# Kernel optimization log

Measured on AMD Instinct MI355X. Metric: run time of the kernel, lower is better.

Reference implementation:

```python
import jax, jax.numpy as jnp
import numpy as np

HID = 256   # hidden_dim
P = 16      # pool_size
EPS = 1e-5


def _ln(x, g, b):
    m = x.mean(-1, keepdims=True)
    v = x.var(-1, keepdims=True)
    return (x - m) * jax.lax.rsqrt(v + EPS) * g + b


def setup_inputs() -> dict:
    key = jax.random.key(0)
    ks = jax.random.split(key, 12)
    B, Cf, H, W = 8, 512, 64, 64
    Cg = Cf // 2
    Co = Cf // 2
    s = 0.02
    d = {}
    d['e_f'] = jax.random.normal(ks[0], (B, Cf, H, W), jnp.float32)
    d['e_g'] = jax.random.normal(ks[1], (B, Cg, H, W), jnp.float32)
    d['l_feat'] = jax.random.normal(ks[2], (B, 768, 20), jnp.float32)
    d['l_mask'] = jnp.ones((B, 20, 1), jnp.float32)
    d['ln_f_g'] = jnp.ones((Cf,), jnp.float32)
    d['ln_f_b'] = jnp.zeros((Cf,), jnp.float32)
    d['ln_g_g'] = jnp.ones((Cg,), jnp.float32)
    d['ln_g_b'] = jnp.zeros((Cg,), jnp.float32)
    d['wq'] = jax.random.normal(ks[3], (Cf, HID), jnp.float32) * s
    d['bq'] = jnp.zeros((HID,), jnp.float32)
    d['wk'] = jax.random.normal(ks[4], (Cg, HID), jnp.float32) * s
    d['bk'] = jnp.zeros((HID,), jnp.float32)
    d['wv'] = jax.random.normal(ks[5], (Cg, HID), jnp.float32) * s
    d['bv'] = jnp.zeros((HID,), jnp.float32)
    d['wo'] = jax.random.normal(ks[6], (HID, HID), jnp.float32) * s
    d['bo'] = jnp.zeros((HID,), jnp.float32)
    d['dw_k'] = jax.random.normal(ks[7], (HID, 1, 3, 3), jnp.float32) * s  # depthwise kernel (OIHW, I=1)
    d['efp_w'] = jax.random.normal(ks[8], (HID, Cf), jnp.float32) * s     # 1x1 conv v_channels->hidden
    d['efp_b'] = jnp.zeros((HID,), jnp.float32)
    d['outc_w'] = jax.random.normal(ks[9], (Co, HID), jnp.float32) * s    # 1x1 conv hidden->out
    d['outc_b'] = jnp.zeros((Co,), jnp.float32)
    d['bn_g'] = jnp.ones((Co,), jnp.float32)
    d['bn_b'] = jnp.zeros((Co,), jnp.float32)
    d['bn_m'] = jnp.zeros((Co,), jnp.float32)
    d['bn_v'] = jnp.ones((Co,), jnp.float32)
    return d


def reference(e_f, e_g, l_feat, l_mask, ln_f_g, ln_f_b, ln_g_g, ln_g_b,
              wq, bq, wk, bk, wv, bv, wo, bo, dw_k, efp_w, efp_b,
              outc_w, outc_b, bn_g, bn_b, bn_m, bn_v):
    B, Cf, H, W = e_f.shape
    # Q = w_qi(LN(e_f))                                  (B, HW, HID)
    q = _ln(e_f.transpose(0, 2, 3, 1), ln_f_g, ln_f_b).reshape(B, H * W, Cf) @ wq + bq
    # K/V projections from LN(e_g)
    g = _ln(e_g.transpose(0, 2, 3, 1), ln_g_g, ln_g_b).reshape(B, H * W, -1)
    k = (g @ wk + bk).reshape(B, H, W, HID)
    v = (g @ wv + bv).reshape(B, H, W, HID)
    # 16x16 max/avg pooling -> (B, Hp*Wp, HID)
    k = jnp.max(k.reshape(B, H // P, P, W // P, P, HID), axis=(2, 4)).reshape(B, -1, HID)
    v = jnp.mean(v.reshape(B, H // P, P, W // P, P, HID), axis=(2, 4)).reshape(B, -1, HID)
    # pooled attention
    attn = jax.nn.softmax(jnp.einsum('bqd,bkd->bqk', q, k) * (HID ** -0.5), axis=-1)
    a_i = jnp.einsum('bqk,bkd->bqd', attn, v)  # (B, HW, HID)
    # depthwise 3x3 conv on Q (NCHW)
    q_nchw = q.reshape(B, H, W, HID).transpose(0, 3, 1, 2)
    dw = jax.lax.conv_general_dilated(q_nchw, dw_k, (1, 1), [(1, 1), (1, 1)],
                                      feature_group_count=HID)
    combined = dw + a_i.reshape(B, H, W, HID).transpose(0, 3, 1, 2)
    comb = combined.transpose(0, 2, 3, 1).reshape(B, H * W, HID) @ wo + bo
    comb = comb.reshape(B, H, W, HID).transpose(0, 3, 1, 2)
    # 1x1 proj of e_f, elementwise gate
    efp = jnp.einsum('bchw,oc->bohw', e_f, efp_w) + efp_b[None, :, None, None]
    e_a = efp * comb
    # out: 1x1 conv + BN (inference) + ReLU (dropout inactive in eval)
    out = jnp.einsum('bchw,oc->bohw', e_a, outc_w) + outc_b[None, :, None, None]
    scale = (bn_g * jax.lax.rsqrt(bn_v + EPS))[None, :, None, None]
    out = (out - bn_m[None, :, None, None]) * scale + bn_b[None, :, None, None]
    return jax.nn.relu(out)
```

## Files before the change

### kernel.cpp

```cpp
#include <hip/hip_runtime.h>
#include <math.h>

#define EPS 1e-5f

typedef __attribute__((ext_vector_type(8))) short bf16x8;
typedef __attribute__((ext_vector_type(4))) float f32x4;

__device__ __forceinline__ unsigned short f2bf(float f) {
    unsigned int u = __float_as_uint(f);
    u += 0x7fff + ((u >> 16) & 1);
    return (unsigned short)(u >> 16);
}
__device__ __forceinline__ float bf2f(unsigned short h) {
    return __uint_as_float(((unsigned int)h) << 16);
}
__device__ __forceinline__ float lof(unsigned int u) {
    return __uint_as_float(u << 16);
}
__device__ __forceinline__ float hif(unsigned int u) {
    return __uint_as_float(u & 0xffff0000u);
}
__device__ __forceinline__ void async16(void* lds, const void* g) {
    __builtin_amdgcn_global_load_lds(
        (const __attribute__((address_space(1))) unsigned int*)g,
        (__attribute__((address_space(3))) unsigned int*)lds, 16, 0, 0);
}

__global__ __launch_bounds__(256) void prep_all(
    const float* __restrict__ lnfg, const float* __restrict__ lnfb,
    const float* __restrict__ wq, const float* __restrict__ bq,
    const float* __restrict__ efpw, const float* __restrict__ efpb,
    const float* __restrict__ lngg, const float* __restrict__ lngb,
    const float* __restrict__ wk, const float* __restrict__ bk,
    const float* __restrict__ wv, const float* __restrict__ bv,
    const float* __restrict__ wo, const float* __restrict__ outcw,
    const float* __restrict__ outcb, const float* __restrict__ bng,
    const float* __restrict__ bnb, const float* __restrict__ bnm,
    const float* __restrict__ bnv, const float* __restrict__ dwk,
    unsigned short* __restrict__ Wb1t, unsigned short* __restrict__ Wb2t,
    unsigned short* __restrict__ Wot, unsigned short* __restrict__ Woc,
    float* __restrict__ dwt,
    float* __restrict__ cs1, float* __restrict__ cst1,
    float* __restrict__ cs2, float* __restrict__ cst2,
    float* __restrict__ scv, float* __restrict__ shv)
{
    int idx = blockIdx.x * 256 + threadIdx.x;
    if (idx < 262144) {
        int n = idx >> 9, k = idx & 511;
        float v = (n < 256) ? lnfg[k] * wq[k * 256 + n]
                            : efpw[(size_t)(n - 256) * 512 + k];
        Wb1t[idx] = f2bf(v);
    } else if (idx < 327680) {
        int j = idx - 262144; int n = j >> 8, k = j & 255;
        Wb2t[j] = f2bf(lngg[k] * wk[k * 256 + n]);
    } else if (idx < 393216) {
        int j = idx - 327680; int n = j >> 8, k = j & 255;
        Wot[j] = f2bf(wo[k * 256 + n]);
    } else if (idx < 458752) {
        int j = idx - 393216;
        Woc[j] = f2bf(outcw[j]);
    } else if (idx < 461056) {
        int j = idx - 458752; int tap = j >> 8, ch = j & 255;
        dwt[j] = dwk[ch * 9 + tap];
    } else if (idx < 462336) {
        int j = idx - 461056;
        if (j < 256) {
            int n = j; float cs = 0.f, ct = 0.f;
            for (int k = 0; k < 512; k++) {
                float w = wq[k * 256 + n];
                cs += lnfg[k] * w; ct += lnfb[k] * w;
            }
            cs1[n] = cs; cst1[n] = ct + bq[n];
        } else if (j < 512) {
            cs1[j] = 0.f; cst1[j] = efpb[j - 256];
        } else if (j < 768) {
            int n = j - 512; float cs = 0.f, ct = 0.f;
            for (int k = 0; k < 256; k++) {
                float w = wk[k * 256 + n];
                cs += lngg[k] * w; ct += lngb[k] * w;
            }
            cs2[n] = cs; cst2[n] = ct + bk[n];
        } else if (j < 1024) {
            int n = j - 768; float cs = 0.f, ct = 0.f;
            for (int k = 0; k < 256; k++) {
                float w = wv[k * 256 + n];
                cs += lngg[k] * w; ct += lngb[k] * w;
            }
            cs2[256 + n] = cs; cst2[256 + n] = ct + bv[n];
        } else {
            int n = j - 1024;
            float s = bng[n] * rsqrtf(bnv[n] + EPS);
            scv[n] = s;
            shv[n] = (outcb[n] - bnm[n]) * s + bnb[n];
        }
    }
}

__global__ __launch_bounds__(256) void transpose_fg(
    const float* __restrict__ ef, const float* __restrict__ eg,
    unsigned short* __restrict__ ef_bf, unsigned short* __restrict__ eg_bf,
    float* __restrict__ pf, float* __restrict__ pfq,
    float* __restrict__ pg, float* __restrict__ pgq)
{
    __shared__ float tile[64][65];
    __shared__ float psum[4][64], pss[4][64];
    int id = blockIdx.x;
    const float* src; unsigned short* dst; float* ps; float* pq;
    int C, cblk, b, p0;
    if (id < 2048) {
        src = ef; dst = ef_bf; ps = pf; pq = pfq; C = 512;
        b = id >> 8; cblk = (id >> 5) & 7; p0 = (id & 31) * 128;
    } else {
        id -= 2048;
        src = eg; dst = eg_bf; ps = pg; pq = pgq; C = 256;
        b = id >> 7; cblk = (id >> 5) & 3; p0 = (id & 31) * 128;
    }
    int c0 = cblk * 64;
    const float* s = src + ((size_t)b * C + c0) * 4096 + p0;
    int t = threadIdx.x;
    int cr = t >> 4, p4 = (t & 15) * 4;
    int lane = t & 63, grp = t >> 6;
    int pr = t >> 3, c8 = (t & 7) * 8;

    float4 r1[4], r2[4];
#pragma unroll
    for (int i = 0; i < 4; i++)
        r1[i] = *(const float4*)(s + (size_t)(i * 16 + cr) * 4096 + p4);
#pragma unroll
    for (int i = 0; i < 4; i++)
        r2[i] = *(const float4*)(s + (size_t)(i * 16 + cr) * 4096 + 64 + p4);

#pragma unroll
    for (int half = 0; half < 2; half++) {
#pragma unroll
        for (int i = 0; i < 4; i++) {
            float4 v = half ? r2[i] : r1[i];
            int c = i * 16 + cr;
            tile[c][p4 + 0] = v.x; tile[c][p4 + 1] = v.y;
            tile[c][p4 + 2] = v.z; tile[c][p4 + 3] = v.w;
        }
        __syncthreads();

        int pbase = p0 + half * 64;
        unsigned short* d = dst + ((size_t)(b * 4096 + pbase)) * C + c0;
#pragma unroll
        for (int i = 0; i < 2; i++) {
            int p = i * 32 + pr;
            uint4 pk;
            pk.x = (unsigned)f2bf(tile[c8 + 0][p]) | ((unsigned)f2bf(tile[c8 + 1][p]) << 16);
            pk.y = (unsigned)f2bf(tile[c8 + 2][p]) | ((unsigned)f2bf(tile[c8 + 3][p]) << 16);
            pk.z = (unsigned)f2bf(tile[c8 + 4][p]) | ((unsigned)f2bf(tile[c8 + 5][p]) << 16);
            pk.w = (unsigned)f2bf(tile[c8 + 6][p]) | ((unsigned)f2bf(tile[c8 + 7][p]) << 16);
            *(uint4*)(d + (size_t)p * C + c8) = pk;
        }

        float sm = 0.f, sq = 0.f;
#pragma unroll
        for (int j = 0; j < 16; j++) {
            float v = tile[grp * 16 + j][lane];
            sm += v; sq += v * v;
        }
        psum[grp][lane] = sm; pss[grp][lane] = sq;
        __syncthreads();
        if (t < 64) {
            float fs = psum[0][t] + psum[1][t] + psum[2][t] + psum[3][t];
            float fq = pss[0][t] + pss[1][t] + pss[2][t] + pss[3][t];
            ps[cblk * 32768 + b * 4096 + pbase + t] = fs;
            pq[cblk * 32768 + b * 4096 + pbase + t] = fq;
        }
        if (half == 0) __syncthreads();
    }
}

__global__ __launch_bounds__(256) void ln_finalize(
    const float* __restrict__ pf, const float* __restrict__ pfq,
    const float* __restrict__ pg, const float* __restrict__ pgq,
    float* __restrict__ mf, float* __restrict__ rf,
    float* __restrict__ mg, float* __restrict__ rg)
{
    int gp = blockIdx.x * 256 + threadIdx.x;
    float s = 0.f, q = 0.f;
#pragma unroll
    for (int i = 0; i < 8; i++) { s += pf[i * 32768 + gp]; q += pfq[i * 32768 + gp]; }
    float m = s * (1.f / 512.f);
    float v = q * (1.f / 512.f) - m * m;
    mf[gp] = m; rf[gp] = rsqrtf(v + EPS);
    s = 0.f; q = 0.f;
#pragma unroll
    for (int i = 0; i < 4; i++) { s += pg[i * 32768 + gp]; q += pgq[i * 32768 + gp]; }
    m = s * (1.f / 256.f);
    v = q * (1.f / 256.f) - m * m;
    mg[gp] = m; rg[gp] = rsqrtf(v + EPS);
}

template<int K>
__device__ __forceinline__ void mfma_core(
    const unsigned short* __restrict__ A, const unsigned short* __restrict__ Bt,
    int m0, int n0, unsigned short* As, unsigned short* Bs, f32x4 acc[4][4])
{
    const int tid = threadIdx.x;
    const int wave = tid >> 6, lane = tid & 63;
    const int wm = (wave & 1) * 64, wn = (wave >> 1) * 64;
#pragma unroll
    for (int i = 0; i < 4; i++)
#pragma unroll
        for (int j = 0; j < 4; j++) acc[i][j] = (f32x4){0.f, 0.f, 0.f, 0.f};

    const int srow = wave * 32 + (lane >> 3);
    const int sg = (lane & 7) ^ ((lane >> 3) & 7);
    const unsigned short* ga = A + (size_t)(m0 + srow) * K + sg * 8;
    const unsigned short* gb = Bt + (size_t)(n0 + srow) * K + sg * 8;

    for (int k0 = 0; k0 < K; k0 += 64) {
#pragma unroll
        for (int t = 0; t < 4; t++) {
            async16(As + (wave * 32 + t * 8) * 64, ga + (size_t)t * 8 * K + k0);
            async16(Bs + (wave * 32 + t * 8) * 64, gb + (size_t)t * 8 * K + k0);
        }
        __syncthreads();
#pragma unroll
        for (int ks = 0; ks < 2; ks++) {
            bf16x8 af[4], bfr[4];
            int kb = ks * 4 + (lane >> 4);
            int slot = (kb ^ (lane & 7)) * 8;
#pragma unroll
            for (int i = 0; i < 4; i++) {
                int m = wm + i * 16 + (lane & 15);
                af[i] = *(const bf16x8*)&As[m * 64 + slot];
                int n = wn + i * 16 + (lane & 15);
                bfr[i] = *(const bf16x8*)&Bs[n * 64 + slot];
            }
#pragma unroll
            for (int i = 0; i < 4; i++)
#pragma unroll
                for (int j = 0; j < 4; j++)
                    acc[i][j] = __builtin_amdgcn_mfma_f32_16x16x32_bf16(
                        af[i], bfr[j], acc[i][j], 0, 0, 0);
        }
        __syncthreads();
    }
}

__global__ __launch_bounds__(256, 2) void gemm1_mfma(
    const unsigned short* __restrict__ ef_bf, const unsigned short* __restrict__ Wb1t,
    const float* __restrict__ cs1, const float* __restrict__ cst1,
    const float* __restrict__ mf, const float* __restrict__ rf,
    unsigned short* __restrict__ qbuf, unsigned short* __restrict__ efpbuf)
{
    __shared__ unsigned short As[128 * 64];
    __shared__ unsigned short Bs[256 * 64];
    f32x4 acc[4][8];
    const int tid = threadIdx.x;
    const int wave = tid >> 6, lane = tid & 63;
    const int wm = (wave & 1) * 64, wn = (wave >> 1) * 128;
    const int m0 = blockIdx.x * 128, n0 = blockIdx.y * 256;
#pragma unroll
    for (int i = 0; i < 4; i++)
#pragma unroll
        for (int j = 0; j < 8; j++) acc[i][j] = (f32x4){0.f, 0.f, 0.f, 0.f};

    const int srow = lane >> 3;
    const int sg = (lane & 7) ^ (srow & 7);
    const unsigned short* ga = ef_bf + (size_t)(m0 + wave * 32 + srow) * 512 + sg * 8;
    const unsigned short* gb = Wb1t + (size_t)(n0 + wave * 64 + srow) * 512 + sg * 8;

    for (int k0 = 0; k0 < 512; k0 += 64) {
#pragma unroll
        for (int t = 0; t < 4; t++)
            async16(As + (wave * 32 + t * 8) * 64, ga + (size_t)t * 8 * 512 + k0);
#pragma unroll
        for (int t = 0; t < 8; t++)
            async16(Bs + (wave * 64 + t * 8) * 64, gb + (size_t)t * 8 * 512 + k0);
        __syncthreads();
#pragma unroll
        for (int ks = 0; ks < 2; ks++) {
            bf16x8 af[4], bfr[8];
            int kb = ks * 4 + (lane >> 4);
            int slot = (kb ^ (lane & 7)) * 8;
#pragma unroll
            for (int i = 0; i < 4; i++)
                af[i] = *(const bf16x8*)&As[(wm + i * 16 + (lane & 15)) * 64 + slot];
#pragma unroll
            for (int j = 0; j < 8; j++)
                bfr[j] = *(const bf16x8*)&Bs[(wn + j * 16 + (lane & 15)) * 64 + slot];
#pragma unroll
            for (int i = 0; i < 4; i++)
#pragma unroll
                for (int j = 0; j < 8; j++)
                    acc[i][j] = __builtin_amdgcn_mfma_f32_16x16x32_bf16(
                        af[i], bfr[j], acc[i][j], 0, 0, 0);
        }
        __syncthreads();
    }

    bool isq = (n0 == 0);
#pragma unroll
    for (int i = 0; i < 4; i++) {
#pragma unroll
        for (int r = 0; r < 4; r++) {
            int gm = m0 + wm + i * 16 + ((lane >> 4) * 4) + r;
            float mean = mf[gm], rs = rf[gm];
#pragma unroll
            for (int j = 0; j < 8; j++) {
                int nn = wn + j * 16 + (lane & 15);
                float v = acc[i][j][r];
                if (isq) {
                    int n = nn;
                    float o = rs * (v - mean * cs1[n]) + cst1[n];
                    qbuf[(size_t)gm * 256 + nn] = f2bf(o);
                } else {
                    int n = nn + 256;
                    efpbuf[(size_t)gm * 256 + nn] = f2bf(v + cst1[n]);
                }
            }
        }
    }
}

__global__ __launch_bounds__(256) void gemm2k_mfma(
    const unsigned short* __restrict__ eg_bf, const unsigned short* __restrict__ Wb2t,
    const float* __restrict__ cs2, const float* __restrict__ cst2,
    const float* __restrict__ mg, const float* __restrict__ rg,
    unsigned short* __restrict__ kfull)
{
    __shared__ unsigned short As[8192], Bs[8192];
    f32x4 acc[4][4];
    int m0 = blockIdx.x * 128, n0 = blockIdx.y * 128;
    mfma_core<256>(eg_bf, Wb2t, m0, n0, As, Bs, acc);
    int lane = threadIdx.x & 63, wave = threadIdx.x >> 6;
    int wm = (wave & 1) * 64, wn = (wave >> 1) * 64;
#pragma unroll
    for (int i = 0; i < 4; i++) {
#pragma unroll
        for (int r = 0; r < 4; r++) {
            int gm = m0 + wm + i * 16 + ((lane >> 4) * 4) + r;
            float mean = mg[gm], rs = rg[gm];
#pragma unroll
            for (int j = 0; j < 4; j++) {
                int n = n0 + wn + j * 16 + (lane & 15);
                float o = rs * (acc[i][j][r] - mean * cs2[n]) + cst2[n];
                kfull[(size_t)gm * 256 + n] = f2bf(o);
            }
        }
    }
}

__global__ __launch_bounds__(256) void gemm34_mfma(
    const unsigned short* __restrict__ comb, const unsigned short* __restrict__ Wot,
    const float* __restrict__ bo, const unsigned short* __restrict__ efp,
    const unsigned short* __restrict__ Woc,
    const float* __restrict__ scv, const float* __restrict__ shv,
    float* __restrict__ outp)
{
    __shared__ unsigned short As[64 * 64];
    __shared__ unsigned short Bs[256 * 64];
    __shared__ unsigned short eat[64 * 256];
    const int tid = threadIdx.x;
    const int wave = tid >> 6, lane = tid & 63;
    const int m0 = blockIdx.x * 64;

    const int srow = lane >> 3;
    const int sg = (lane & 7) ^ (srow & 7);

    f32x4 acc[4][4];
#pragma unroll
    for (int i = 0; i < 4; i++)
#pragma unroll
        for (int j = 0; j < 4; j++) acc[i][j] = (f32x4){0.f, 0.f, 0.f, 0.f};

    const unsigned short* ga = comb + (size_t)(m0 + wave * 16 + srow) * 256 + sg * 8;
    const unsigned short* gb = Wot + (size_t)(wave * 64 + srow) * 256 + sg * 8;

    for (int k0 = 0; k0 < 256; k0 += 64) {
#pragma unroll
        for (int t = 0; t < 2; t++)
            async16(As + (wave * 16 + t * 8) * 64, ga + (size_t)t * 8 * 256 + k0);
#pragma unroll
        for (int t = 0; t < 8; t++)
            async16(Bs + (wave * 64 + t * 8) * 64, gb + (size_t)t * 8 * 256 + k0);
        __syncthreads();
#pragma unroll
        for (int ks = 0; ks < 2; ks++) {
            bf16x8 af[4], bfr[4];
            int kb = ks * 4 + (lane >> 4);
            int slot = (kb ^ (lane & 7)) * 8;
#pragma unroll
            for (int i = 0; i < 4; i++) {
                af[i]  = *(const bf16x8*)&As[(i * 16 + (lane & 15)) * 64 + slot];
                bfr[i] = *(const bf16x8*)&Bs[(wave * 64 + i * 16 + (lane & 15)) * 64 + slot];
            }
#pragma unroll
            for (int i = 0; i < 4; i++)
#pragma unroll
                for (int j = 0; j < 4; j++)
                    acc[i][j] = __builtin_amdgcn_mfma_f32_16x16x32_bf16(
                        af[i], bfr[j], acc[i][j], 0, 0, 0);
        }
        __syncthreads();
    }

    float bo4[4];
#pragma unroll
    for (int j = 0; j < 4; j++) bo4[j] = bo[wave * 64 + j * 16 + (lane & 15)];
#pragma unroll
    for (int i = 0; i < 4; i++) {
#pragma unroll
        for (int r = 0; r < 4; r++) {
            int pos = i * 16 + ((lane >> 4) * 4) + r;
#pragma unroll
            for (int j = 0; j < 4; j++) {
                int n = wave * 64 + j * 16 + (lane & 15);
                float o = (acc[i][j][r] + bo4[j])
                          * bf2f(efp[(size_t)(m0 + pos) * 256 + n]);
                int o8 = j * 2 + ((lane >> 3) & 1);
                int slot = o8 ^ (pos & 7);
                eat[pos * 256 + wave * 64 + slot * 8 + (lane & 7)] = f2bf(o);
            }
        }
    }

    f32x4 acc2[4][4];
#pragma unroll
    for (int i = 0; i < 4; i++)
#pragma unroll
        for (int j = 0; j < 4; j++) acc2[i][j] = (f32x4){0.f, 0.f, 0.f, 0.f};

    const unsigned short* gw = Woc + (size_t)(wave * 64 + srow) * 256 + sg * 8;
    for (int k0 = 0; k0 < 256; k0 += 64) {
#pragma unroll
        for (int t = 0; t < 8; t++)
            async16(Bs + (wave * 64 + t * 8) * 64, gw + (size_t)t * 8 * 256 + k0);
        __syncthreads();
        int kc = k0 >> 6;
#pragma unroll
        for (int ks = 0; ks < 2; ks++) {
            bf16x8 af2[4], bf2_[4];
            int kb = ks * 4 + (lane >> 4);
            int slot = (kb ^ (lane & 7)) * 8;
#pragma unroll
            for (int i = 0; i < 4; i++) {
                af2[i]  = *(const bf16x8*)&Bs[(wave * 64 + i * 16 + (lane & 15)) * 64 + slot];
                bf2_[i] = *(const bf16x8*)&eat[(i * 16 + (lane & 15)) * 256 + kc * 64 + slot];
            }
#pragma unroll
            for (int i = 0; i < 4; i++)
#pragma unroll
                for (int j = 0; j < 4; j++)
                    acc2[i][j] = __builtin_amdgcn_mfma_f32_16x16x32_bf16(
                        af2[i], bf2_[j], acc2[i][j], 0, 0, 0);
        }
        __syncthreads();
    }

#pragma unroll
    for (int i = 0; i < 4; i++) {
#pragma unroll
        for (int r = 0; r < 4; r++) {
            int co = wave * 64 + i * 16 + ((lane >> 4) * 4) + r;
            float s = scv[co], hh = shv[co];
#pragma unroll
            for (int j = 0; j < 4; j++) {
                int p = m0 + j * 16 + (lane & 15);
                float o = fmaxf(fmaf(acc2[i][j][r], s, hh), 0.f);
                outp[((size_t)(p >> 12)) * 1048576 + (size_t)co * 4096 + (p & 4095)] = o;
            }
        }
    }
}

__global__ __launch_bounds__(256) void pool_phase(
    const unsigned short* __restrict__ kfull, const float* __restrict__ eg,
    const float* __restrict__ rg, const float* __restrict__ mg,
    unsigned short* __restrict__ kpb, float* __restrict__ s1,
    float* __restrict__ s0)
{
    __shared__ float smem[4352];
    int id = blockIdx.x;
    int t = threadIdx.x;
    if (id < 128) {
        int b = id >> 4, cell = id & 15;
        int hp = cell >> 2, wp = cell & 3;
        int g8 = t & 31, rr = t >> 5;
        float kmx[8];
#pragma unroll
        for (int j = 0; j < 8; j++) kmx[j] = -3.402823466e38f;
#pragma unroll
        for (int rsub = 0; rsub < 2; rsub++) {
            int r = rr * 2 + rsub;
            int prow = (hp * 16 + r) * 64 + wp * 16;
            for (int cl = 0; cl < 16; cl++) {
                size_t basei = ((size_t)(b * 4096 + prow + cl)) * 256 + g8 * 8;
                uint4 kv = *(const uint4*)(kfull + basei);
                kmx[0] = fmaxf(kmx[0], lof(kv.x)); kmx[1] = fmaxf(kmx[1], hif(kv.x));
                kmx[2] = fmaxf(kmx[2], lof(kv.y)); kmx[3] = fmaxf(kmx[3], hif(kv.y));
                kmx[4] = fmaxf(kmx[4], lof(kv.z)); kmx[5] = fmaxf(kmx[5], hif(kv.z));
                kmx[6] = fmaxf(kmx[6], lof(kv.w)); kmx[7] = fmaxf(kmx[7], hif(kv.w));
            }
// ... 129 lines not shown
        int hh = h + dy - 1;
        if (hh < 0 || hh > 63) continue;
        const unsigned short* qr = qbuf + ((size_t)(b * 4096 + hh * 64)) * 256;
        float4 ft[6];
#pragma unroll
        for (int c = 0; c < 6; c++) {
            int xx = w0 - 1 + c;
            if (xx < 0 || xx > 63) {
                ft[c] = (float4){0.f, 0.f, 0.f, 0.f};
            } else {
                uint2 qa = *(const uint2*)(qr + (size_t)xx * 256 + o4);
                ft[c] = (float4){lof(qa.x), hif(qa.x), lof(qa.y), hif(qa.y)};
            }
        }
#pragma unroll
        for (int dx = 0; dx < 3; dx++) {
            float4 kk = kreg[dy * 3 + dx];
#pragma unroll
            for (int i = 0; i < 4; i++) {
                float4 qv = ft[i + dx];
                acc[i].x = fmaf(qv.x, kk.x, acc[i].x);
                acc[i].y = fmaf(qv.y, kk.y, acc[i].y);
                acc[i].z = fmaf(qv.z, kk.z, acc[i].z);
                acc[i].w = fmaf(qv.w, kk.w, acc[i].w);
            }
        }
    }
#pragma unroll
    for (int i = 0; i < 4; i++) {
        uint2 pk;
        pk.x = (unsigned)f2bf(acc[i].x) | ((unsigned)f2bf(acc[i].y) << 16);
        pk.y = (unsigned)f2bf(acc[i].z) | ((unsigned)f2bf(acc[i].w) << 16);
        *(uint2*)(combined + ((size_t)(b * 4096 + pidx + i)) * 256 + o4) = pk;
    }
}

extern "C" void kernel_launch(void* const* d_in, const int* in_sizes, int n_in,
                              void* d_out, int out_size, void* d_ws, size_t ws_size,
                              hipStream_t stream)
{
    const float* e_f   = (const float*)d_in[0];
    const float* e_g   = (const float*)d_in[1];
    const float* lnfg  = (const float*)d_in[4];
    const float* lnfb  = (const float*)d_in[5];
    const float* lngg  = (const float*)d_in[6];
    const float* lngb  = (const float*)d_in[7];
    const float* wq    = (const float*)d_in[8];
    const float* bq    = (const float*)d_in[9];
    const float* wk    = (const float*)d_in[10];
    const float* bk    = (const float*)d_in[11];
    const float* wv    = (const float*)d_in[12];
    const float* bv    = (const float*)d_in[13];
    const float* wo    = (const float*)d_in[14];
    const float* bo    = (const float*)d_in[15];
    const float* dwk   = (const float*)d_in[16];
    const float* efpw  = (const float*)d_in[17];
    const float* efpb  = (const float*)d_in[18];
    const float* outcw = (const float*)d_in[19];
    const float* outcb = (const float*)d_in[20];
    const float* bng   = (const float*)d_in[21];
    const float* bnb   = (const float*)d_in[22];
    const float* bnm   = (const float*)d_in[23];
    const float* bnv   = (const float*)d_in[24];
    float* outp = (float*)d_out;

    char* base = (char*)d_ws;
    auto alloc = [&](size_t bytes) -> char* {
        char* r = base; base += (bytes + 255) & ~(size_t)255; return r;
    };
    float* pf    = (float*)alloc(8 * 32768 * 4);
    float* pfq   = (float*)alloc(8 * 32768 * 4);
    float* pg    = (float*)alloc(4 * 32768 * 4);
    float* pgq   = (float*)alloc(4 * 32768 * 4);
    float* mf    = (float*)alloc(32768 * 4);
    float* rf    = (float*)alloc(32768 * 4);
    float* mg    = (float*)alloc(32768 * 4);
    float* rg    = (float*)alloc(32768 * 4);
    float* cs1   = (float*)alloc(512 * 4);
    float* cst1  = (float*)alloc(512 * 4);
    float* cs2   = (float*)alloc(512 * 4);
    float* cst2  = (float*)alloc(512 * 4);
    float* scv   = (float*)alloc(256 * 4);
    float* shv   = (float*)alloc(256 * 4);
    float* dwt   = (float*)alloc(9 * 256 * 4);
    unsigned short* Wb1t = (unsigned short*)alloc(262144 * 2);
    unsigned short* Wb2t = (unsigned short*)alloc(65536 * 2);
    unsigned short* Wot  = (unsigned short*)alloc(65536 * 2);
    unsigned short* Woc  = (unsigned short*)alloc(65536 * 2);
    unsigned short* ef_bf = (unsigned short*)alloc((size_t)32768 * 512 * 2);
    unsigned short* eg_bf = (unsigned short*)alloc((size_t)32768 * 256 * 2);
    unsigned short* qbuf  = (unsigned short*)alloc((size_t)32768 * 256 * 2);
    unsigned short* efpbuf = (unsigned short*)alloc((size_t)32768 * 256 * 2);
    unsigned short* kfull = (unsigned short*)alloc((size_t)32768 * 256 * 2);
    unsigned short* kpb  = (unsigned short*)alloc(128 * 256 * 2);
    float* vp    = (float*)alloc(128 * 256 * 4);
    float* s1    = (float*)alloc(128 * 256 * 4);
    float* s0    = (float*)alloc(128 * 4);

    prep_all<<<1806, 256, 0, stream>>>(
        lnfg, lnfb, wq, bq, efpw, efpb, lngg, lngb, wk, bk, wv, bv, wo,
        outcw, outcb, bng, bnb, bnm, bnv, dwk,
        Wb1t, Wb2t, Wot, Woc, dwt, cs1, cst1, cs2, cst2, scv, shv);
    transpose_fg<<<3072, 256, 0, stream>>>(e_f, e_g, ef_bf, eg_bf,
                                           pf, pfq, pg, pgq);
    ln_finalize<<<128, 256, 0, stream>>>(pf, pfq, pg, pgq, mf, rf, mg, rg);
    gemm1_mfma<<<dim3(256, 2), 256, 0, stream>>>(ef_bf, Wb1t, cs1, cst1, mf, rf,
                                                 qbuf, efpbuf);
    gemm2k_mfma<<<dim3(256, 2), 256, 0, stream>>>(eg_bf, Wb2t, cs2, cst2, mg, rg,
                                                  kfull);
    pool_phase<<<640, 256, 0, stream>>>(kfull, e_g, rg, mg, kpb, s1, s0);
    vpool_gemm<<<128, 256, 0, stream>>>(s1, s0, lngg, wv, cs2, cst2, vp);
    combined_dw<<<2048, 256, 0, stream>>>(qbuf, kpb, vp, dwt, kfull);
    gemm34_mfma<<<512, 256, 0, stream>>>(kfull, Wot, bo, efpbuf,
                                         Woc, scv, shv, outp);
}
```

Measured before the change: 316.7 us.

## Merge prep with transpose, fold LN finalize into GEMMs, and merge projection GEMMs

Weight prep and the input transpose/stat pass now run in a single launch with block-index dispatch. The separate LN-finalize kernel is removed: each projection GEMM block reduces the partial sums for its own rows into shared memory, and the K-GEMM still writes mg/rg for later kernels. The Q/efp GEMM and the K GEMM are merged into one 1024-block launch. This saves launches and inter-kernel gaps, at the cost of a fatter kernel whose register and LDS use is sized for the heavier branch.

Measured after the change: 311.5 us. No clear change (-1.7%).

```diff
diff --git a/kernel.cpp b/kernel.cpp
--- a/kernel.cpp
+++ b/kernel.cpp
@@ -26,7 +26,11 @@
         (__attribute__((address_space(3))) unsigned int*)lds, 16, 0, 0);
 }
 
-__global__ __launch_bounds__(256) void prep_all(
+__global__ __launch_bounds__(256) void trans_prep(
+    const float* __restrict__ ef, const float* __restrict__ eg,
+    unsigned short* __restrict__ ef_bf, unsigned short* __restrict__ eg_bf,
+    float* __restrict__ pf, float* __restrict__ pfq,
+    float* __restrict__ pg, float* __restrict__ pgq,
     const float* __restrict__ lnfg, const float* __restrict__ lnfb,
     const float* __restrict__ wq, const float* __restrict__ bq,
     const float* __restrict__ efpw, const float* __restrict__ efpb,
@@ -44,153 +48,127 @@
     float* __restrict__ cs2, float* __restrict__ cst2,
     float* __restrict__ scv, float* __restrict__ shv)
 {
-    int idx = blockIdx.x * 256 + threadIdx.x;
-    if (idx < 262144) {
-        int n = idx >> 9, k = idx & 511;
-        float v = (n < 256) ? lnfg[k] * wq[k * 256 + n]
-                            : efpw[(size_t)(n - 256) * 512 + k];
-        Wb1t[idx] = f2bf(v);
-    } else if (idx < 327680) {
-        int j = idx - 262144; int n = j >> 8, k = j & 255;
-        Wb2t[j] = f2bf(lngg[k] * wk[k * 256 + n]);
-    } else if (idx < 393216) {
-        int j = idx - 327680; int n = j >> 8, k = j & 255;
-        Wot[j] = f2bf(wo[k * 256 + n]);
-    } else if (idx < 458752) {
-        int j = idx - 393216;
-        Woc[j] = f2bf(outcw[j]);
-    } else if (idx < 461056) {
-        int j = idx - 458752; int tap = j >> 8, ch = j & 255;
-        dwt[j] = dwk[ch * 9 + tap];
-    } else if (idx < 462336) {
-        int j = idx - 461056;
-        if (j < 256) {
-            int n = j; float cs = 0.f, ct = 0.f;
-            for (int k = 0; k < 512; k++) {
-                float w = wq[k * 256 + n];
-                cs += lnfg[k] * w; ct += lnfb[k] * w;
-            }
-            cs1[n] = cs; cst1[n] = ct + bq[n];
-        } else if (j < 512) {
-            cs1[j] = 0.f; cst1[j] = efpb[j - 256];
-        } else if (j < 768) {
-            int n = j - 512; float cs = 0.f, ct = 0.f;
-            for (int k = 0; k < 256; k++) {
-                float w = wk[k * 256 + n];
-                cs += lngg[k] * w; ct += lngb[k] * w;
-            }
-            cs2[n] = cs; cst2[n] = ct + bk[n];
-        } else if (j < 1024) {
-            int n = j - 768; float cs = 0.f, ct = 0.f;
-            for (int k = 0; k < 256; k++) {
-                float w = wv[k * 256 + n];
-                cs += lngg[k] * w; ct += lngb[k] * w;
-            }
-            cs2[256 + n] = cs; cst2[256 + n] = ct + bv[n];
-        } else {
-            int n = j - 1024;
-            float s = bng[n] * rsqrtf(bnv[n] + EPS);
-            scv[n] = s;
-            shv[n] = (outcb[n] - bnm[n]) * s + bnb[n];
-        }
-    }
-}
-
-__global__ __launch_bounds__(256) void transpose_fg(
-    const float* __restrict__ ef, const float* __restrict__ eg,
-    unsigned short* __restrict__ ef_bf, unsigned short* __restrict__ eg_bf,
-    float* __restrict__ pf, float* __restrict__ pfq,
-    float* __restrict__ pg, float* __restrict__ pgq)
-{
     __shared__ float tile[64][65];
     __shared__ float psum[4][64], pss[4][64];
     int id = blockIdx.x;
-    const float* src; unsigned short* dst; float* ps; float* pq;
-    int C, cblk, b, p0;
-    if (id < 2048) {
-        src = ef; dst = ef_bf; ps = pf; pq = pfq; C = 512;
-        b = id >> 8; cblk = (id >> 5) & 7; p0 = (id & 31) * 128;
+    if (id < 3072) {
+        const float* src; unsigned short* dst; float* ps; float* pq;
+        int C, cblk, b, p0;
+        if (id < 2048) {
+            src = ef; dst = ef_bf; ps = pf; pq = pfq; C = 512;
+            b = id >> 8; cblk = (id >> 5) & 7; p0 = (id & 31) * 128;
+        } else {
+            id -= 2048;
+            src = eg; dst = eg_bf; ps = pg; pq = pgq; C = 256;
+            b = id >> 7; cblk = (id >> 5) & 3; p0 = (id & 31) * 128;
+        }
+        int c0 = cblk * 64;
+        const float* s = src + ((size_t)b * C + c0) * 4096 + p0;
+        int t = threadIdx.x;
+        int cr = t >> 4, p4 = (t & 15) * 4;
+        int lane = t & 63, grp = t >> 6;
+        int pr = t >> 3, c8 = (t & 7) * 8;
+
+        float4 r1[4], r2[4];
+#pragma unroll
+        for (int i = 0; i < 4; i++)
+            r1[i] = *(const float4*)(s + (size_t)(i * 16 + cr) * 4096 + p4);
+#pragma unroll
+        for (int i = 0; i < 4; i++)
+            r2[i] = *(const float4*)(s + (size_t)(i * 16 + cr) * 4096 + 64 + p4);
+
+#pragma unroll
+        for (int half = 0; half < 2; half++) {
+#pragma unroll
+            for (int i = 0; i < 4; i++) {
+                float4 v = half ? r2[i] : r1[i];
+                int c = i * 16 + cr;
+                tile[c][p4 + 0] = v.x; tile[c][p4 + 1] = v.y;
+                tile[c][p4 + 2] = v.z; tile[c][p4 + 3] = v.w;
+            }
+            __syncthreads();
+
+            int pbase = p0 + half * 64;
+            unsigned short* d = dst + ((size_t)(b * 4096 + pbase)) * C + c0;
+#pragma unroll
+            for (int i = 0; i < 2; i++) {
+                int p = i * 32 + pr;
+                uint4 pk;
+                pk.x = (unsigned)f2bf(tile[c8 + 0][p]) | ((unsigned)f2bf(tile[c8 + 1][p]) << 16);
+                pk.y = (unsigned)f2bf(tile[c8 + 2][p]) | ((unsigned)f2bf(tile[c8 + 3][p]) << 16);
+                pk.z = (unsigned)f2bf(tile[c8 + 4][p]) | ((unsigned)f2bf(tile[c8 + 5][p]) << 16);
+                pk.w = (unsigned)f2bf(tile[c8 + 6][p]) | ((unsigned)f2bf(tile[c8 + 7][p]) << 16);
+                *(uint4*)(d + (size_t)p * C + c8) = pk;
+            }
+
+            float sm = 0.f, sq = 0.f;
+#pragma unroll
+            for (int j = 0; j < 16; j++) {
+                float v = tile[grp * 16 + j][lane];
+                sm += v; sq += v * v;
+            }
+            psum[grp][lane] = sm; pss[grp][lane] = sq;
+            __syncthreads();
+            if (t < 64) {
+                float fs = psum[0][t] + psum[1][t] + psum[2][t] + psum[3][t];
+                float fq = pss[0][t] + pss[1][t] + pss[2][t] + pss[3][t];
+                ps[cblk * 32768 + b * 4096 + pbase + t] = fs;
+                pq[cblk * 32768 + b * 4096 + pbase + t] = fq;
+            }
+            if (half == 0) __syncthreads();
+        }
     } else {
-        id -= 2048;
-        src = eg; dst = eg_bf; ps = pg; pq = pgq; C = 256;
-        b = id >> 7; cblk = (id >> 5) & 3; p0 = (id & 31) * 128;
-    }
-    int c0 = cblk * 64;
-    const float* s = src + ((size_t)b * C + c0) * 4096 + p0;
-    int t = threadIdx.x;
-    int cr = t >> 4, p4 = (t & 15) * 4;
-    int lane = t & 63, grp = t >> 6;
-    int pr = t >> 3, c8 = (t & 7) * 8;
-
-    float4 r1[4], r2[4];
-#pragma unroll
-    for (int i = 0; i < 4; i++)
-        r1[i] = *(const float4*)(s + (size_t)(i * 16 + cr) * 4096 + p4);
-#pragma unroll
-    for (int i = 0; i < 4; i++)
-        r2[i] = *(const float4*)(s + (size_t)(i * 16 + cr) * 4096 + 64 + p4);
-
-#pragma unroll
-    for (int half = 0; half < 2; half++) {
-#pragma unroll
-        for (int i = 0; i < 4; i++) {
-            float4 v = half ? r2[i] : r1[i];
-            int c = i * 16 + cr;
-            tile[c][p4 + 0] = v.x; tile[c][p4 + 1] = v.y;
-            tile[c][p4 + 2] = v.z; tile[c][p4 + 3] = v.w;
-        }
-        __syncthreads();
-
-        int pbase = p0 + half * 64;
-        unsigned short* d = dst + ((size_t)(b * 4096 + pbase)) * C + c0;
-#pragma unroll
-        for (int i = 0; i < 2; i++) {
-            int p = i * 32 + pr;
-            uint4 pk;
-            pk.x = (unsigned)f2bf(tile[c8 + 0][p]) | ((unsigned)f2bf(tile[c8 + 1][p]) << 16);
-            pk.y = (unsigned)f2bf(tile[c8 + 2][p]) | ((unsigned)f2bf(tile[c8 + 3][p]) << 16);
-            pk.z = (unsigned)f2bf(tile[c8 + 4][p]) | ((unsigned)f2bf(tile[c8 + 5][p]) << 16);
-            pk.w = (unsigned)f2bf(tile[c8 + 6][p]) | ((unsigned)f2bf(tile[c8 + 7][p]) << 16);
-            *(uint4*)(d + (size_t)p * C + c8) = pk;
-        }
-
-        float sm = 0.f, sq = 0.f;
-#pragma unroll
-        for (int j = 0; j < 16; j++) {
-            float v = tile[grp * 16 + j][lane];
-            sm += v; sq += v * v;
-        }
-        psum[grp][lane] = sm; pss[grp][lane] = sq;
-        __syncthreads();
-        if (t < 64) {
-            float fs = psum[0][t] + psum[1][t] + psum[2][t] + psum[3][t];
-            float fq = pss[0][t] + pss[1][t] + pss[2][t] + pss[3][t];
-            ps[cblk * 32768 + b * 4096 + pbase + t] = fs;
-            pq[cblk * 32768 + b * 4096 + pbase + t] = fq;
-        }
-        if (half == 0) __syncthreads();
-    }
-}
-
-__global__ __launch_bounds__(256) void ln_finalize(
-    const float* __restrict__ pf, const float* __restrict__ pfq,
-    const float* __restrict__ pg, const float* __restrict__ pgq,
-    float* __restrict__ mf, float* __restrict__ rf,
-    float* __restrict__ mg, float* __restrict__ rg)
-{
-    int gp = blockIdx.x * 256 + threadIdx.x;
-    float s = 0.f, q = 0.f;
-#pragma unroll
-    for (int i = 0; i < 8; i++) { s += pf[i * 32768 + gp]; q += pfq[i * 32768 + gp]; }
-    float m = s * (1.f / 512.f);
-    float v = q * (1.f / 512.f) - m * m;
-    mf[gp] = m; rf[gp] = rsqrtf(v + EPS);
-    s = 0.f; q = 0.f;
-#pragma unroll
-    for (int i = 0; i < 4; i++) { s += pg[i * 32768 + gp]; q += pgq[i * 32768 + gp]; }
-    m = s * (1.f / 256.f);
-    v = q * (1.f / 256.f) - m * m;
-    mg[gp] = m; rg[gp] = rsqrtf(v + EPS);
+        int idx = (id - 3072) * 256 + threadIdx.x;
+        if (idx < 262144) {
+            int n = idx >> 9, k = idx & 511;
+            float v = (n < 256) ? lnfg[k] * wq[k * 256 + n]
+                                : efpw[(size_t)(n - 256) * 512 + k];
+            Wb1t[idx] = f2bf(v);
+        } else if (idx < 327680) {
+            int j = idx - 262144; int n = j >> 8, k = j & 255;
+            Wb2t[j] = f2bf(lngg[k] * wk[k * 256 + n]);
+        } else if (idx < 393216) {
+            int j = idx - 327680; int n = j >> 8, k = j & 255;
+            Wot[j] = f2bf(wo[k * 256 + n]);
+        } else if (idx < 458752) {
+            int j = idx - 393216;
+            Woc[j] = f2bf(outcw[j]);
+        } else if (idx < 461056) {
+            int j = idx - 458752; int tap = j >> 8, ch = j & 255;
+            dwt[j] = dwk[ch * 9 + tap];
+        } else if (idx < 462336) {
+            int j = idx - 461056;
+            if (j < 256) {
+                int n = j; float cs = 0.f, ct = 0.f;
+                for (int k = 0; k < 512; k++) {
+                    float w = wq[k * 256 + n];
+                    cs += lnfg[k] * w; ct += lnfb[k] * w;
+                }
+                cs1[n] = cs; cst1[n] = ct + bq[n];
+            } else if (j < 512) {
+                cs1[j] = 0.f; cst1[j] = efpb[j - 256];
+            } else if (j < 768) {
+                int n = j - 512; float cs = 0.f, ct = 0.f;
+                for (int k = 0; k < 256; k++) {
+                    float w = wk[k * 256 + n];
+                    cs += lngg[k] * w; ct += lngb[k] * w;
+                }
+                cs2[n] = cs; cst2[n] = ct + bk[n];
+            } else if (j < 1024) {
+                int n = j - 768; float cs = 0.f, ct = 0.f;
+                for (int k = 0; k < 256; k++) {
+                    float w = wv[k * 256 + n];
+                    cs += lngg[k] * w; ct += lngb[k] * w;
+                }
+                cs2[256 + n] = cs; cst2[256 + n] = ct + bv[n];
+            } else {
+                int n = j - 1024;
+                float s = bng[n] * rsqrtf(bnv[n] + EPS);
+                scv[n] = s;
+                shv[n] = (outcb[n] - bnm[n]) * s + bnb[n];
+            }
+        }
+    }
 }
 
 template<int K>
@@ -241,228 +219,132 @@
     }
 }
 
-__global__ __launch_bounds__(256, 2) void gemm1_mfma(
+__global__ __launch_bounds__(256, 2) void gemm_proj(
     const unsigned short* __restrict__ ef_bf, const unsigned short* __restrict__ Wb1t,
     const float* __restrict__ cs1, const float* __restrict__ cst1,
-    const float* __restrict__ mf, const float* __restrict__ rf,
-    unsigned short* __restrict__ qbuf, unsigned short* __restrict__ efpbuf)
+    const float* __restrict__ pf, const float* __restrict__ pfq,
+    unsigned short* __restrict__ qbuf, unsigned short* __restrict__ efpbuf,
+    const unsigned short* __restrict__ eg_bf, const unsigned short* __restrict__ Wb2t,
+    const float* __restrict__ cs2, const float* __restrict__ cst2,
+    const float* __restrict__ pg, const float* __restrict__ pgq,
+    float* __restrict__ mg, float* __restrict__ rg,
+    unsigned short* __restrict__ kfull)
 {
     __shared__ unsigned short As[128 * 64];
     __shared__ unsigned short Bs[256 * 64];
-    f32x4 acc[4][8];
+    __shared__ float sstat[256];
     const int tid = threadIdx.x;
     const int wave = tid >> 6, lane = tid & 63;
-    const int wm = (wave & 1) * 64, wn = (wave >> 1) * 128;
-    const int m0 = blockIdx.x * 128, n0 = blockIdx.y * 256;
-#pragma unroll
-    for (int i = 0; i < 4; i++)
-#pragma unroll
-        for (int j = 0; j < 8; j++) acc[i][j] = (f32x4){0.f, 0.f, 0.f, 0.f};
-
-    const int srow = lane >> 3;
-    const int sg = (lane & 7) ^ (srow & 7);
-    const unsigned short* ga = ef_bf + (size_t)(m0 + wave * 32 + srow) * 512 + sg * 8;
-    const unsigned short* gb = Wb1t + (size_t)(n0 + wave * 64 + srow) * 512 + sg * 8;
-
-    for (int k0 = 0; k0 < 512; k0 += 64) {
-#pragma unroll
-        for (int t = 0; t < 4; t++)
-            async16(As + (wave * 32 + t * 8) * 64, ga + (size_t)t * 8 * 512 + k0);
-#pragma unroll
-        for (int t = 0; t < 8; t++)
-            async16(Bs + (wave * 64 + t * 8) * 64, gb + (size_t)t * 8 * 512 + k0);
-        __syncthreads();
-#pragma unroll
-        for (int ks = 0; ks < 2; ks++) {
-            bf16x8 af[4], bfr[8];
-            int kb = ks * 4 + (lane >> 4);
-            int slot = (kb ^ (lane & 7)) * 8;
-#pragma unroll
-            for (int i = 0; i < 4; i++)
-                af[i] = *(const bf16x8*)&As[(wm + i * 16 + (lane & 15)) * 64 + slot];
-#pragma unroll
-            for (int j = 0; j < 8; j++)
-                bfr[j] = *(const bf16x8*)&Bs[(wn + j * 16 + (lane & 15)) * 64 + slot];
-#pragma unroll
-            for (int i = 0; i < 4; i++)
+    const int bid = blockIdx.x;
+
+    if (bid < 512) {
+        const int m0 = (bid >> 1) * 128, n0 = (bid & 1) * 256;
+        const int wm = (wave & 1) * 64, wn = (wave >> 1) * 128;
+        f32x4 acc[4][8];
+
+        if (tid < 128) {
+            int gm = m0 + tid;
+            float s = 0.f, q = 0.f;
+#pragma unroll
+            for (int i = 0; i < 8; i++) { s += pf[i * 32768 + gm]; q += pfq[i * 32768 + gm]; }
+            float m = s * (1.f / 512.f);
+            sstat[tid] = m;
+            sstat[128 + tid] = rsqrtf(q * (1.f / 512.f) - m * m + EPS);
+        }
+
+#pragma unroll
+        for (int i = 0; i < 4; i++)
+#pragma unroll
+            for (int j = 0; j < 8; j++) acc[i][j] = (f32x4){0.f, 0.f, 0.f, 0.f};
+
+        const int srow = lane >> 3;
+        const int sg = (lane & 7) ^ (srow & 7);
+        const unsigned short* ga = ef_bf + (size_t)(m0 + wave * 32 + srow) * 512 + sg * 8;
+        const unsigned short* gb = Wb1t + (size_t)(n0 + wave * 64 + srow) * 512 + sg * 8;
+
+        for (int k0 = 0; k0 < 512; k0 += 64) {
+#pragma unroll
+            for (int t = 0; t < 4; t++)
+                async16(As + (wave * 32 + t * 8) * 64, ga + (size_t)t * 8 * 512 + k0);
+#pragma unroll
+            for (int t = 0; t < 8; t++)
+                async16(Bs + (wave * 64 + t * 8) * 64, gb + (size_t)t * 8 * 512 + k0);
+            __syncthreads();
+#pragma unroll
+            for (int ks = 0; ks < 2; ks++) {
+                bf16x8 af[4], bfr[8];
+                int kb = ks * 4 + (lane >> 4);
+                int slot = (kb ^ (lane & 7)) * 8;
+#pragma unroll
+                for (int i = 0; i < 4; i++)
+                    af[i] = *(const bf16x8*)&As[(wm + i * 16 + (lane & 15)) * 64 + slot];
 #pragma unroll
                 for (int j = 0; j < 8; j++)
-                    acc[i][j] = __builtin_amdgcn_mfma_f32_16x16x32_bf16(
-                        af[i], bfr[j], acc[i][j], 0, 0, 0);
-        }
-        __syncthreads();
-    }
-
-    bool isq = (n0 == 0);
-#pragma unroll
-    for (int i = 0; i < 4; i++) {
-#pragma unroll
-        for (int r = 0; r < 4; r++) {
-            int gm = m0 + wm + i * 16 + ((lane >> 4) * 4) + r;
-            float mean = mf[gm], rs = rf[gm];
-#pragma unroll
-            for (int j = 0; j < 8; j++) {
-                int nn = wn + j * 16 + (lane & 15);
-                float v = acc[i][j][r];
-                if (isq) {
-                    int n = nn;
-                    float o = rs * (v - mean * cs1[n]) + cst1[n];
-                    qbuf[(size_t)gm * 256 + nn] = f2bf(o);
-                } else {
-                    int n = nn + 256;
-                    efpbuf[(size_t)gm * 256 + nn] = f2bf(v + cst1[n]);
+                    bfr[j] = *(const bf16x8*)&Bs[(wn + j * 16 + (lane & 15)) * 64 + slot];
+#pragma unroll
+                for (int i = 0; i < 4; i++)
+#pragma unroll
+                    for (int j = 0; j < 8; j++)
+                        acc[i][j] = __builtin_amdgcn_mfma_f32_16x16x32_bf16(
+                            af[i], bfr[j], acc[i][j], 0, 0, 0);
+            }
+            __syncthreads();
+        }
+
+        bool isq = (n0 == 0);
+#pragma unroll
+        for (int i = 0; i < 4; i++) {
+#pragma unroll
+            for (int r = 0; r < 4; r++) {
+                int lm = wm + i * 16 + ((lane >> 4) * 4) + r;
+                int gm = m0 + lm;
+                float mean = sstat[lm], rs = sstat[128 + lm];
+#pragma unroll
+                for (int j = 0; j < 8; j++) {
+                    int nn = wn + j * 16 + (lane & 15);
+                    float v = acc[i][j][r];
+                    if (isq) {
+                        int n = nn;
+                        float o = rs * (v - mean * cs1[n]) + cst1[n];
+                        qbuf[(size_t)gm * 256 + nn] = f2bf(o);
+                    } else {
+                        int n = nn + 256;
+                        efpbuf[(size_t)gm * 256 + nn] = f2bf(v + cst1[n]);
+                    }
                 }
             }
         }
-    }
-}
-
-__global__ __launch_bounds__(256) void gemm2k_mfma(
-    const unsigned short* __restrict__ eg_bf, const unsigned short* __restrict__ Wb2t,
-    const float* __restrict__ cs2, const float* __restrict__ cst2,
-    const float* __restrict__ mg, const float* __restrict__ rg,
-    unsigned short* __restrict__ kfull)
-{
-    __shared__ unsigned short As[8192], Bs[8192];
-    f32x4 acc[4][4];
-    int m0 = blockIdx.x * 128, n0 = blockIdx.y * 128;
-    mfma_core<256>(eg_bf, Wb2t, m0, n0, As, Bs, acc);
-    int lane = threadIdx.x & 63, wave = threadIdx.x >> 6;
-    int wm = (wave & 1) * 64, wn = (wave >> 1) * 64;
-#pragma unroll
-    for (int i = 0; i < 4; i++) {
-#pragma unroll
-        for (int r = 0; r < 4; r++) {
-            int gm = m0 + wm + i * 16 + ((lane >> 4) * 4) + r;
-            float mean = mg[gm], rs = rg[gm];
-#pragma unroll
-            for (int j = 0; j < 4; j++) {
-                int n = n0 + wn + j * 16 + (lane & 15);
-                float o = rs * (acc[i][j][r] - mean * cs2[n]) + cst2[n];
-                kfull[(size_t)gm * 256 + n] = f2bf(o);
-            }
-        }
-    }
-}
-
-__global__ __launch_bounds__(256) void gemm34_mfma(
-    const unsigned short* __restrict__ comb, const unsigned short* __restrict__ Wot,
-    const float* __restrict__ bo, const unsigned short* __restrict__ efp,
-    const unsigned short* __restrict__ Woc,
-    const float* __restrict__ scv, const float* __restrict__ shv,
-    float* __restrict__ outp)
-{
-    __shared__ unsigned short As[64 * 64];
-    __shared__ unsigned short Bs[256 * 64];
-    __shared__ unsigned short eat[64 * 256];
-    const int tid = threadIdx.x;
-    const int wave = tid >> 6, lane = tid & 63;
-    const int m0 = blockIdx.x * 64;
-
-    const int srow = lane >> 3;
-    const int sg = (lane & 7) ^ (srow & 7);
-
-    f32x4 acc[4][4];
-#pragma unroll
-    for (int i = 0; i < 4; i++)
-#pragma unroll
-        for (int j = 0; j < 4; j++) acc[i][j] = (f32x4){0.f, 0.f, 0.f, 0.f};
-
-    const unsigned short* ga = comb + (size_t)(m0 + wave * 16 + srow) * 256 + sg * 8;
-    const unsigned short* gb = Wot + (size_t)(wave * 64 + srow) * 256 + sg * 8;
-
-    for (int k0 = 0; k0 < 256; k0 += 64) {
-#pragma unroll
-        for (int t = 0; t < 2; t++)
-            async16(As + (wave * 16 + t * 8) * 64, ga + (size_t)t * 8 * 256 + k0);
-#pragma unroll
-        for (int t = 0; t < 8; t++)
-            async16(Bs + (wave * 64 + t * 8) * 64, gb + (size_t)t * 8 * 256 + k0);
-        __syncthreads();
-#pragma unroll
-        for (int ks = 0; ks < 2; ks++) {
-            bf16x8 af[4], bfr[4];
-            int kb = ks * 4 + (lane >> 4);
-            int slot = (kb ^ (lane & 7)) * 8;
-#pragma unroll
-            for (int i = 0; i < 4; i++) {
-                af[i]  = *(const bf16x8*)&As[(i * 16 + (lane & 15)) * 64 + slot];
-                bfr[i] = *(const bf16x8*)&Bs[(wave * 64 + i * 16 + (lane & 15)) * 64 + slot];
-            }
-#pragma unroll
-            for (int i = 0; i < 4; i++)
-#pragma unroll
-                for (int j = 0; j < 4; j++)
-                    acc[i][j] = __builtin_amdgcn_mfma_f32_16x16x32_bf16(
-                        af[i], bfr[j], acc[i][j], 0, 0, 0);
-        }
-        __syncthreads();
-    }
-
-    float bo4[4];
-#pragma unroll
-    for (int j = 0; j < 4; j++) bo4[j] = bo[wave * 64 + j * 16 + (lane & 15)];
-#pragma unroll
-    for (int i = 0; i < 4; i++) {
-#pragma unroll
-        for (int r = 0; r < 4; r++) {
-            int pos = i * 16 + ((lane >> 4) * 4) + r;
-#pragma unroll
-            for (int j = 0; j < 4; j++) {
-                int n = wave * 64 + j * 16 + (lane & 15);
-                float o = (acc[i][j][r] + bo4[j])
-                          * bf2f(efp[(size_t)(m0 + pos) * 256 + n]);
-                int o8 = j * 2 + ((lane >> 3) & 1);
-                int slot = o8 ^ (pos & 7);
-                eat[pos * 256 + wave * 64 + slot * 8 + (lane & 7)] = f2bf(o);
-            }
-        }
-    }
-
-    f32x4 acc2[4][4];
-#pragma unroll
-    for (int i = 0; i < 4; i++)
-#pragma unroll
-        for (int j = 0; j < 4; j++) acc2[i][j] = (f32x4){0.f, 0.f, 0.f, 0.f};
-
-    const unsigned short* gw = Woc + (size_t)(wave * 64 + srow) * 256 + sg * 8;
-    for (int k0 = 0; k0 < 256; k0 += 64) {
-#pragma unroll
-        for (int t = 0; t < 8; t++)
-            async16(Bs + (wave * 64 + t * 8) * 64, gw + (size_t)t * 8 * 256 + k0);
-        __syncthreads();
-        int kc = k0 >> 6;
-#pragma unroll
-        for (int ks = 0; ks < 2; ks++) {
-            bf16x8 af2[4], bf2_[4];
-            int kb = ks * 4 + (lane >> 4);
-            int slot = (kb ^ (lane & 7)) * 8;
-#pragma unroll
-            for (int i = 0; i < 4; i++) {
-                af2[i]  = *(const bf16x8*)&Bs[(wave * 64 + i * 16 + (lane & 15)) * 64 + slot];
-                bf2_[i] = *(const bf16x8*)&eat[(i * 16 + (lane & 15)) * 256 + kc * 64 + slot];
-            }
-#pragma unroll
-            for (int i = 0; i < 4; i++)
-#pragma unroll
-                for (int j = 0; j < 4; j++)
-                    acc2[i][j] = __builtin_amdgcn_mfma_f32_16x16x32_bf16(
-                        af2[i], bf2_[j], acc2[i][j], 0, 0, 0);
-        }
-        __syncthreads();
-    }
-
-#pragma unroll
-    for (int i = 0; i < 4; i++) {
-#pragma unroll
-        for (int r = 0; r < 4; r++) {
-            int co = wave * 64 + i * 16 + ((lane >> 4) * 4) + r;
-            float s = scv[co], hh = shv[co];
-#pragma unroll
-            for (int j = 0; j < 4; j++) {
-                int p = m0 + j * 16 + (lane & 15);
-                float o = fmaxf(fmaf(acc2[i][j][r], s, hh), 0.f);
-                outp[((size_t)(p >> 12)) * 1048576 + (size_t)co * 4096 + (p & 4095)] = o;
+    } else {
+        const int j2 = bid - 512;
+        const int m0 = (j2 >> 1) * 128, n0 = (j2 & 1) * 128;
+        f32x4 acc[4][4];
+
+        if (tid < 128) {
+            int gm = m0 + tid;
+            float s = 0.f, q = 0.f;
+#pragma unroll
+            for (int i = 0; i < 4; i++) { s += pg[i * 32768 + gm]; q += pgq[i * 32768 + gm]; }
+            float m = s * (1.f / 256.f);
+            float r = rsqrtf(q * (1.f / 256.f) - m * m + EPS);
+            sstat[tid] = m; sstat[128 + tid] = r;
+            if (n0 == 0) { mg[gm] = m; rg[gm] = r; }
+        }
+
+        mfma_core<256>(eg_bf, Wb2t, m0, n0, As, Bs, acc);
+        int wm = (wave & 1) * 64, wn = (wave >> 1) * 64;
+#pragma unroll
+        for (int i = 0; i < 4; i++) {
+#pragma unroll
+            for (int r = 0; r < 4; r++) {
+                int lm = wm + i * 16 + ((lane >> 4) * 4) + r;
+                int gm = m0 + lm;
+                float mean = sstat[lm], rs = sstat[128 + lm];
+#pragma unroll
+                for (int j = 0; j < 4; j++) {
+                    int n = n0 + wn + j * 16 + (lane & 15);
+                    float o = rs * (acc[i][j][r] - mean * cs2[n]) + cst2[n];
+                    kfull[(size_t)gm * 256 + n] = f2bf(o);
+                }
             }
         }
     }
@@ -658,6 +540,129 @@
         pk.x = (unsigned)f2bf(acc[i].x) | ((unsigned)f2bf(acc[i].y) << 16);
         pk.y = (unsigned)f2bf(acc[i].z) | ((unsigned)f2bf(acc[i].w) << 16);
         *(uint2*)(combined + ((size_t)(b * 4096 + pidx + i)) * 256 + o4) = pk;
+    }
+}
+
+__global__ __launch_bounds__(256) void gemm34_mfma(
+    const unsigned short* __restrict__ comb, const unsigned short* __restrict__ Wot,
+    const float* __restrict__ bo, const unsigned short* __restrict__ efp,
+    const unsigned short* __restrict__ Woc,
+    const float* __restrict__ scv, const float* __restrict__ shv,
+    float* __restrict__ outp)
+{
+    __shared__ unsigned short As[64 * 64];
+    __shared__ unsigned short Bs[256 * 64];
+    __shared__ unsigned short eat[64 * 256];
+    const int tid = threadIdx.x;
+    const int wave = tid >> 6, lane = tid & 63;
+    const int m0 = blockIdx.x * 64;
+
+    const int srow = lane >> 3;
+    const int sg = (lane & 7) ^ (srow & 7);
+
+    f32x4 acc[4][4];
+#pragma unroll
+    for (int i = 0; i < 4; i++)
+#pragma unroll
+        for (int j = 0; j < 4; j++) acc[i][j] = (f32x4){0.f, 0.f, 0.f, 0.f};
+
+    const unsigned short* ga = comb + (size_t)(m0 + wave * 16 + srow) * 256 + sg * 8;
+    const unsigned short* gb = Wot + (size_t)(wave * 64 + srow) * 256 + sg * 8;
+
+    for (int k0 = 0; k0 < 256; k0 += 64) {
+#pragma unroll
+        for (int t = 0; t < 2; t++)
+            async16(As + (wave * 16 + t * 8) * 64, ga + (size_t)t * 8 * 256 + k0);
+#pragma unroll
+        for (int t = 0; t < 8; t++)
+            async16(Bs + (wave * 64 + t * 8) * 64, gb + (size_t)t * 8 * 256 + k0);
+        __syncthreads();
+#pragma unroll
+        for (int ks = 0; ks < 2; ks++) {
+            bf16x8 af[4], bfr[4];
+            int kb = ks * 4 + (lane >> 4);
+            int slot = (kb ^ (lane & 7)) * 8;
+#pragma unroll
+            for (int i = 0; i < 4; i++) {
+                af[i]  = *(const bf16x8*)&As[(i * 16 + (lane & 15)) * 64 + slot];
+                bfr[i] = *(const bf16x8*)&Bs[(wave * 64 + i * 16 + (lane & 15)) * 64 + slot];
+            }
+#pragma unroll
+            for (int i = 0; i < 4; i++)
+#pragma unroll
+                for (int j = 0; j < 4; j++)
+                    acc[i][j] = __builtin_amdgcn_mfma_f32_16x16x32_bf16(
+                        af[i], bfr[j], acc[i][j], 0, 0, 0);
+        }
+        __syncthreads();
+    }
+
+    float bo4[4];
+#pragma unroll
+    for (int j = 0; j < 4; j++) bo4[j] = bo[wave * 64 + j * 16 + (lane & 15)];
+#pragma unroll
+    for (int i = 0; i < 4; i++) {
+#pragma unroll
+        for (int r = 0; r < 4; r++) {
+            int pos = i * 16 + ((lane >> 4) * 4) + r;
+#pragma unroll
+            for (int j = 0; j < 4; j++) {
+                int n = wave * 64 + j * 16 + (lane & 15);
+                float o = (acc[i][j][r] + bo4[j])
+                          * bf2f(efp[(size_t)(m0 + pos) * 256 + n]);
+                int o8 = j * 2 + ((lane >> 3) & 1);
+                int slot = o8 ^ (pos & 7);
+                eat[pos * 256 + wave * 64 + slot * 8 + (lane & 7)] = f2bf(o);
+            }
+        }
+    }
+
+    f32x4 acc2[4][4];
+#pragma unroll
+    for (int i = 0; i < 4; i++)
+#pragma unroll
+        for (int j = 0; j < 4; j++) acc2[i][j] = (f32x4){0.f, 0.f, 0.f, 0.f};
+
+    const unsigned short* gw = Woc + (size_t)(wave * 64 + srow) * 256 + sg * 8;
+    for (int k0 = 0; k0 < 256; k0 += 64) {
+#pragma unroll
+        for (int t = 0; t < 8; t++)
+            async16(Bs + (wave * 64 + t * 8) * 64, gw + (size_t)t * 8 * 256 + k0);
+        __syncthreads();
+        int kc = k0 >> 6;
+#pragma unroll
+        for (int ks = 0; ks < 2; ks++) {
+            bf16x8 af2[4], bf2_[4];
+            int kb = ks * 4 + (lane >> 4);
+            int slot = (kb ^ (lane & 7)) * 8;
+#pragma unroll
+            for (int i = 0; i < 4; i++) {
+                af2[i]  = *(const bf16x8*)&Bs[(wave * 64 + i * 16 + (lane & 15)) * 64 + slot];
+                bf2_[i] = *(const bf16x8*)&eat[(i * 16 + (lane & 15)) * 256 + kc * 64 + slot];
+            }
+#pragma unroll
+            for (int i = 0; i < 4; i++)
+#pragma unroll
+                for (int j = 0; j < 4; j++)
+                    acc2[i][j] = __builtin_amdgcn_mfma_f32_16x16x32_bf16(
+                        af2[i], bf2_[j], acc2[i][j], 0, 0, 0);
+        }
+        __syncthreads();
+    }
+
+#pragma unroll
+    for (int i = 0; i < 4; i++) {
+#pragma unroll
+        for (int r = 0; r < 4; r++) {
+            int co = wave * 64 + i * 16 + ((lane >> 4) * 4) + r;
+            float s = scv[co], hh = shv[co];
+#pragma unroll
+            for (int j = 0; j < 4; j++) {
+                int p = m0 + j * 16 + (lane & 15);
+                float o = fmaxf(fmaf(acc2[i][j][r], s, hh), 0.f);
+                outp[((size_t)(p >> 12)) * 1048576 + (size_t)co * 4096 + (p & 4095)] = o;
+            }
+        }
     }
 }
 
@@ -698,8 +703,6 @@
     float* pfq   = (float*)alloc(8 * 32768 * 4);
     float* pg    = (float*)alloc(4 * 32768 * 4);
     float* pgq   = (float*)alloc(4 * 32768 * 4);
-    float* mf    = (float*)alloc(32768 * 4);
-    float* rf    = (float*)alloc(32768 * 4);
     float* mg    = (float*)alloc(32768 * 4);
     float* rg    = (float*)alloc(32768 * 4);
     float* cs1   = (float*)alloc(512 * 4);
@@ -723,17 +726,14 @@
     float* s1    = (float*)alloc(128 * 256 * 4);
     float* s0    = (float*)alloc(128 * 4);
 
-    prep_all<<<1806, 256, 0, stream>>>(
+    trans_prep<<<4878, 256, 0, stream>>>(
+        e_f, e_g, ef_bf, eg_bf, pf, pfq, pg, pgq,
         lnfg, lnfb, wq, bq, efpw, efpb, lngg, lngb, wk, bk, wv, bv, wo,
         outcw, outcb, bng, bnb, bnm, bnv, dwk,
         Wb1t, Wb2t, Wot, Woc, dwt, cs1, cst1, cs2, cst2, scv, shv);
-    transpose_fg<<<3072, 256, 0, stream>>>(e_f, e_g, ef_bf, eg_bf,
-                                           pf, pfq, pg, pgq);
-    ln_finalize<<<128, 256, 0, stream>>>(pf, pfq, pg, pgq, mf, rf, mg, rg);
-    gemm1_mfma<<<dim3(256, 2), 256, 0, stream>>>(ef_bf, Wb1t, cs1, cst1, mf, rf,
-                                                 qbuf, efpbuf);
-    gemm2k_mfma<<<dim3(256, 2), 256, 0, stream>>>(eg_bf, Wb2t, cs2, cst2, mg, rg,
-                                                  kfull);
+    gemm_proj<<<1024, 256, 0, stream>>>(
+        ef_bf, Wb1t, cs1, cst1, pf, pfq, qbuf, efpbuf,
+        eg_bf, Wb2t, cs2, cst2, pg, pgq, mg, rg, kfull);
     pool_phase<<<640, 256, 0, stream>>>(kfull, e_g, rg, mg, kpb, s1, s0);
     vpool_gemm<<<128, 256, 0, stream>>>(s1, s0, lngg, wv, cs2, cst2, vp);
     combined_dw<<<2048, 256, 0, stream>>>(qbuf, kpb, vp, dwt, kfull);
```
